# Performance work log

Measured on AMD Instinct MI355X. Metric: run time of the kernel, lower is better.

## Reference

```python
import jax, jax.numpy as jnp
import numpy as np
import math

D_MODEL = 1024
N_HEADS = 16
D_HEAD = D_MODEL // N_HEADS
MAX_SEQ_LEN = 2048
BASE = 10000.0


def _rope_tables(L):
    pos = jnp.arange(L, dtype=jnp.float32)[:, None]                      # [L,1]
    freqs = jnp.exp(-math.log(BASE) * jnp.arange(0, D_HEAD, 2, dtype=jnp.float32) / D_HEAD)  # [d/2]
    angles = pos * freqs                                                  # [L, d/2]
    return jnp.sin(angles), jnp.cos(angles)


def _apply_rope(x, sin, cos):
    # x: [B, L, H, d_head], interleaved even/odd rotation
    s = sin[None, :, None, :]
    c = cos[None, :, None, :]
    x_even, x_odd = x[..., ::2], x[..., 1::2]
    rot_even = x_even * c - x_odd * s
    rot_odd = x_even * s + x_odd * c
    # re-interleave: stack on new last axis then flatten
    return jnp.stack([rot_even, rot_odd], axis=-1).reshape(x.shape)


def setup_inputs() -> dict:
    key = jax.random.key(0)
    k0, k1, k2, k3, k4 = jax.random.split(key, 5)
    B, L = 2, 2048
    scale = 1.0 / math.sqrt(D_MODEL)
    return {
        "x": jax.random.normal(k0, (B, L, D_MODEL), dtype=jnp.float32),
        "W_q": jax.random.normal(k1, (D_MODEL, D_MODEL), dtype=jnp.float32) * scale,
        "W_k": jax.random.normal(k2, (D_MODEL, D_MODEL), dtype=jnp.float32) * scale,
        "W_v": jax.random.normal(k3, (D_MODEL, D_MODEL), dtype=jnp.float32) * scale,
        "W_o": jax.random.normal(k4, (D_MODEL, D_MODEL), dtype=jnp.float32) * scale,
    }


def reference(x, W_q, W_k, W_v, W_o):
    B, L, _ = x.shape
    sin, cos = _rope_tables(L)
    # nn.Linear(no bias): y = x @ W.T
    q = (x @ W_q.T).reshape(B, L, N_HEADS, D_HEAD)
    k = (x @ W_k.T).reshape(B, L, N_HEADS, D_HEAD)
    v = (x @ W_v.T).reshape(B, L, N_HEADS, D_HEAD)
    q = _apply_rope(q, sin, cos)
    k = _apply_rope(k, sin, cos)
    scores = jnp.einsum('blhd,bshd->bhls', q, k) / math.sqrt(D_HEAD)
    weights = jax.nn.softmax(scores, axis=-1)
    out = jnp.einsum('bhls,bshd->blhd', weights, v).reshape(B, L, D_MODEL)
    return out @ W_o.T
```

## Files before the change

kernel.cpp:

```cpp
#include <hip/hip_runtime.h>
#include <hip/hip_bf16.h>
#include <math.h>

typedef __bf16 bf16_t;
typedef __bf16 bf16x8 __attribute__((ext_vector_type(8)));
typedef __bf16 bf16x4 __attribute__((ext_vector_type(4)));
typedef float  f32x4  __attribute__((ext_vector_type(4)));
typedef float  f32x16 __attribute__((ext_vector_type(16)));
typedef unsigned u32x4 __attribute__((ext_vector_type(4)));

#define D_MODEL 1024
#define NH      16
#define DH      64
#define LSEQ    2048
#define NROWS   4096
#define LOG2E   1.44269504088896340736f
#define SHIFT_L2 17.312340490667562f

__device__ __forceinline__ void gld_lds16(bf16_t* lds, const bf16_t* g) {
  __builtin_amdgcn_global_load_lds(
      (__attribute__((address_space(1))) void*)(unsigned long long)g,
      (__attribute__((address_space(3))) void*)lds,
      16, 0, 0);
}

__device__ __forceinline__ unsigned cvtpk_bf16(float lo, float hi) {
  unsigned r;
  asm("v_cvt_pk_bf16_f32 %0, %1, %2" : "=v"(r) : "v"(lo), "v"(hi));
  return r;
}

__device__ __forceinline__ void pl32swap(unsigned& a, unsigned& b) {
  asm volatile("v_permlane32_swap_b32 %0, %1" : "+v"(a), "+v"(b));
}

__global__ __launch_bounds__(256)
void k_prep(const float* __restrict__ x,
            const float* __restrict__ w0, const float* __restrict__ w1,
            const float* __restrict__ w2, const float* __restrict__ w3,
            bf16_t* __restrict__ xb, bf16_t* __restrict__ wout, float2* __restrict__ tab)
{
  int gid = blockIdx.x * 256 + threadIdx.x;
  if (gid < 1048576) {
    float4 v = ((const float4*)x)[gid];
    bf16x4 o = { (bf16_t)v.x, (bf16_t)v.y, (bf16_t)v.z, (bf16_t)v.w };
    ((bf16x4*)xb)[gid] = o;
  } else if (gid < 2097152) {
    int i = gid - 1048576;
    int src = i >> 18;
    const float* w = (src == 0) ? w0 : (src == 1) ? w1 : (src == 2) ? w2 : w3;
    float4 v = ((const float4*)w)[i & 262143];
    bf16x4 o = { (bf16_t)v.x, (bf16_t)v.y, (bf16_t)v.z, (bf16_t)v.w };
    ((bf16x4*)wout)[i] = o;
  } else if (gid < 2162688) {
    int i = gid - 2097152;
    int l = i >> 5, p = i & 31;
    float freq = expf(-0.28782313662425575f * (float)p);
    float s, c;
    sincosf((float)l * freq, &s, &c);
    tab[i] = make_float2(c, s);
  }
}

template<int MODE>
__global__ __launch_bounds__(512, 6)
void k_gemm(const bf16_t* __restrict__ A, const bf16_t* __restrict__ B,
            int N, int K,
            float* __restrict__ Fo,
            bf16_t* __restrict__ Qo, bf16_t* __restrict__ Ko, bf16_t* __restrict__ Vo,
            const float2* __restrict__ tab)
{
  __shared__ bf16_t As[3][128 * 32];
  __shared__ bf16_t Bs[3][128 * 32];
  const int tid  = threadIdx.x;
  const int wave = tid >> 6, lane = tid & 63;
  const int hi   = lane >> 4, lo = lane & 15;
  const int m0   = blockIdx.y * 128, n0 = blockIdx.x * 128;
  const int wr2  = (wave >> 1) * 32, wc2 = (wave & 1) * 64;

  const int srow = tid >> 2, sslot = tid & 3;
  const bf16_t* Ap = A + (size_t)(m0 + srow) * K + (sslot ^ ((srow >> 1) & 3)) * 8;
  const bf16_t* Bp = B + (size_t)(n0 + srow) * K + (sslot ^ ((srow >> 1) & 3)) * 8;

  auto stage = [&](int buf) {
    gld_lds16(&As[buf][tid * 8], Ap);
    gld_lds16(&Bs[buf][tid * 8], Bp);
    Ap += 32; Bp += 32;
  };

  const int s16 = (hi ^ ((lo >> 1) & 3)) * 8;

  f32x4 acc[2][4] = {};

  auto compute = [&](int buf) {
    bf16x8 a[2], b[4];
    #pragma unroll
    for (int mi = 0; mi < 2; mi++)
      a[mi] = *(const bf16x8*)(&As[buf][(wr2 + mi * 16 + lo) * 32 + s16]);
    #pragma unroll
    for (int ni = 0; ni < 4; ni++)
      b[ni] = *(const bf16x8*)(&Bs[buf][(wc2 + ni * 16 + lo) * 32 + s16]);
    __builtin_amdgcn_s_setprio(1);
    #pragma unroll
    for (int mi = 0; mi < 2; mi++)
      #pragma unroll
      for (int ni = 0; ni < 4; ni++)
        acc[mi][ni] = __builtin_amdgcn_mfma_f32_16x16x32_bf16(a[mi], b[ni], acc[mi][ni], 0, 0, 0);
    __builtin_amdgcn_s_setprio(0);
  };

  const int nt = K >> 5;
  stage(0);
  stage(1);
  #pragma unroll 1
  for (int t = 0; t < nt - 2; ++t) {
    asm volatile("s_waitcnt vmcnt(2)" ::: "memory");
    __builtin_amdgcn_sched_barrier(0);
    __builtin_amdgcn_s_barrier();
    __builtin_amdgcn_sched_barrier(0);
    stage((t + 2) % 3);
    compute(t % 3);
  }
  asm volatile("s_waitcnt vmcnt(2)" ::: "memory");
  __builtin_amdgcn_sched_barrier(0);
  __builtin_amdgcn_s_barrier();
  __builtin_amdgcn_sched_barrier(0);
  compute((nt - 2) % 3);
  asm volatile("s_waitcnt vmcnt(0)" ::: "memory");
  __builtin_amdgcn_sched_barrier(0);
  __builtin_amdgcn_s_barrier();
  __builtin_amdgcn_sched_barrier(0);
  compute((nt - 1) % 3);

  if constexpr (MODE == 0) {
    #pragma unroll
    for (int mi = 0; mi < 2; mi++)
      #pragma unroll
      for (int ni = 0; ni < 4; ni++)
        #pragma unroll
        for (int r = 0; r < 4; r++) {
          int row = m0 + wr2 + mi * 16 + hi * 4 + r;
          int col = n0 + wc2 + ni * 16 + lo;
          Fo[(size_t)row * N + col] = acc[mi][ni][r];
        }
  } else {
    #pragma unroll
    for (int mi = 0; mi < 2; mi++)
      #pragma unroll
      for (int ni = 0; ni < 4; ni++)
        #pragma unroll
        for (int r = 0; r < 4; r++) {
          float val  = acc[mi][ni][r];
          float part = __shfl_xor(val, 1, 64);
          int row = m0 + wr2 + mi * 16 + hi * 4 + r;
          int col = n0 + wc2 + ni * 16 + lo;
          int which = col >> 10;
          int h = (col >> 6) & 15;
          int d = col & 63;
          int b = row >> 11, l = row & 2047;
          size_t oidx = ((size_t)(b * NH + h) * LSEQ + l) * DH + d;
          if (which == 2) {
            Vo[oidx] = (bf16_t)val;
          } else {
            float2 sc = tab[l * 32 + (d >> 1)];
            float rot = (d & 1) ? (part * sc.y + val * sc.x) : (val * sc.x - part * sc.y);
            if (which == 0) rot *= 0.125f * LOG2E;
            (which == 0 ? Qo : Ko)[oidx] = (bf16_t)rot;
          }
        }
  }
}

__global__ __launch_bounds__(256)
void k_vt(const bf16_t* __restrict__ Vrm, bf16_t* __restrict__ VT) {
  __shared__ bf16_t T[64][66];
  const int tid = threadIdx.x;
  const int bh = blockIdx.y, l0 = blockIdx.x * 64;
  const bf16_t* src = Vrm + ((size_t)bh * LSEQ + l0) * DH;
  #pragma unroll
  for (int pass = 0; pass < 2; pass++) {
    int chunk = tid + pass * 256;
    int row = chunk >> 3, slot = chunk & 7;
    bf16x8 v = *(const bf16x8*)(src + row * DH + slot * 8);
    #pragma unroll
    for (int j = 0; j < 8; j++) T[slot * 8 + j][row] = v[j];
  }
  __syncthreads();
  bf16_t* dst = VT + (size_t)bh * DH * LSEQ + l0;
  #pragma unroll
  for (int pass = 0; pass < 2; pass++) {
    int chunk = tid + pass * 256;
    int d = chunk >> 3, slot = chunk & 7;
    bf16x8 v;
    #pragma unroll
    for (int j = 0; j < 8; j++) v[j] = T[d][slot * 8 + j];
    *(bf16x8*)(dst + (size_t)d * LSEQ + slot * 8) = v;
  }
}

__global__ __launch_bounds__(1024)
void k_attn(const bf16_t* __restrict__ Q, const bf16_t* __restrict__ K,
            const bf16_t* __restrict__ VT, bf16_t* __restrict__ O)
{
  __shared__ __align__(16) bf16_t smem[49152];
  const int tid  = threadIdx.x;
  const int wave = tid >> 6, lane = tid & 63;
  const int kg   = wave & 1;
  const int qg   = wave >> 1;
  const int ql   = lane & 31;
  const int hi   = lane >> 5;
  const int bh = blockIdx.x;
  const int qblock = blockIdx.y * 256 + qg * 32;

  bf16_t* kbase = smem + kg * 3 * 4096;
  bf16_t* vbase = smem + 24576 + kg * 3 * 4096;

  const bf16_t* Qb = Q + (size_t)bh * LSEQ * DH;

  bf16x8 qf[4];
  #pragma unroll
  for (int s = 0; s < 4; s++)
    qf[s] = *(const bf16x8*)(Qb + (size_t)(qblock + ql) * DH + s * 16 + hi * 8);

  const int r0 = qg * 8 + (lane >> 3), s0l = lane & 7;
  const int swo = (s0l ^ (r0 & 7)) * 8;
  const bf16_t* kgp = K  + ((size_t)bh * LSEQ + kg * 1024 + r0) * DH + swo;
  const bf16_t* vgp = VT + ((size_t)bh * DH + r0) * LSEQ + kg * 1024 + swo;
  const int dstoff = qg * 512 + lane * 8;

  auto stage = [&](int buf) {
    gld_lds16(kbase + buf * 4096 + dstoff, kgp);
    gld_lds16(vbase + buf * 4096 + dstoff, vgp);
    kgp += 64 * DH; vgp += 64;
  };

  f32x16 acc[2] = {};
  float lrun = 0.f;

  f32x16 shinit;
  #pragma unroll
  for (int r = 0; r < 16; r++) shinit[r] = -SHIFT_L2;

  auto compute = [&](const bf16_t* Kbuf, const bf16_t* Vbuf) {
    const char* Kcur = (const char*)Kbuf;
    f32x16 st[2] = { shinit, shinit };
    __builtin_amdgcn_s_setprio(1);
    #pragma unroll
    for (int kt = 0; kt < 2; kt++) {
      int row = kt * 32 + ql;
      int swz = (row & 7) << 4;
      #pragma unroll
      for (int s = 0; s < 4; s++) {
        bf16x8 ka = *(const bf16x8*)(Kcur + row * 128 + ((s * 32 + hi * 16) ^ swz));
        st[kt] = __builtin_amdgcn_mfma_f32_32x32x16_bf16(ka, qf[s], st[kt], 0, 0, 0);
      }
    }
    __builtin_amdgcn_s_setprio(0);

    float p[32];
    float rs = 0.f;
    #pragma unroll
    for (int kt = 0; kt < 2; kt++)
      #pragma unroll
      for (int r = 0; r < 16; r++) {
        float e = __builtin_amdgcn_exp2f(st[kt][r]);
        p[kt * 16 + r] = e;
        rs += e;
      }
    lrun += rs;

    bf16x8 pa[4];
    #pragma unroll
    for (int g = 0; g < 4; g++) {
      unsigned a0 = cvtpk_bf16(p[g * 8 + 0], p[g * 8 + 1]);
      unsigned b0 = cvtpk_bf16(p[g * 8 + 4], p[g * 8 + 5]);
      pl32swap(a0, b0);
      unsigned a1 = cvtpk_bf16(p[g * 8 + 2], p[g * 8 + 3]);
      unsigned b1 = cvtpk_bf16(p[g * 8 + 6], p[g * 8 + 7]);
      pl32swap(a1, b1);
      union { u32x4 u; bf16x8 h; } w;
      w.u[0] = a0; w.u[1] = a1; w.u[2] = b0; w.u[3] = b1;
      pa[g] = w.h;
    }

    const char* Vcur = (const char*)Vbuf;
    __builtin_amdgcn_s_setprio(1);
    #pragma unroll
    for (int dt = 0; dt < 2; dt++) {
      int row = dt * 32 + ql;
      int swz = (row & 7) << 4;
      #pragma unroll
      for (int ks = 0; ks < 4; ks++) {
        bf16x8 va = *(const bf16x8*)(Vcur + row * 128 + ((ks * 32 + hi * 16) ^ swz));
        acc[dt] = __builtin_amdgcn_mfma_f32_32x32x16_bf16(va, pa[ks], acc[dt], 0, 0, 0);
      }
    }
    __builtin_amdgcn_s_setprio(0);
  };

  stage(0);
  stage(1);
  #pragma unroll 1
  for (int t = 0; t < 14; ++t) {
    asm volatile("s_waitcnt vmcnt(2)" ::: "memory");
    __builtin_amdgcn_sched_barrier(0);
    __builtin_amdgcn_s_barrier();
    __builtin_amdgcn_sched_barrier(0);
    stage((t + 2) % 3);
    compute(kbase + (t % 3) * 4096, vbase + (t % 3) * 4096);
  }
  asm volatile("s_waitcnt vmcnt(2)" ::: "memory");
  __builtin_amdgcn_sched_barrier(0);
  __builtin_amdgcn_s_barrier();
  __builtin_amdgcn_sched_barrier(0);
  compute(kbase + 2 * 4096, vbase + 2 * 4096);
  asm volatile("s_waitcnt vmcnt(0)" ::: "memory");
  __builtin_amdgcn_sched_barrier(0);
  __builtin_amdgcn_s_barrier();
  __builtin_amdgcn_sched_barrier(0);
  compute(kbase, vbase);

  __syncthreads();
  float* xch = (float*)smem;
  float* px = xch + (qg * 64 + lane) * 34;
  if (kg == 1) {
    #pragma unroll
    for (int r = 0; r < 16; r++) { px[r] = acc[0][r]; px[16 + r] = acc[1][r]; }
    px[32] = lrun;
  }
  __syncthreads();
  if (kg == 0) {
    #pragma unroll
    for (int r = 0; r < 16; r++) { acc[0][r] += px[r]; acc[1][r] += px[16 + r]; }
    lrun += px[32];
    float lfull = lrun + __shfl_xor(lrun, 32, 64);
    float inv = 1.0f / lfull;
    const int b = bh >> 4, h = bh & 15;
    const int lpos = qblock + ql;
    #pragma unroll
    for (int dt = 0; dt < 2; dt++)
      #pragma unroll
      for (int r = 0; r < 16; r++) {
        int d = dt * 32 + (r & 3) + 8 * (r >> 2) + 4 * hi;
        O[(size_t)(b * LSEQ + lpos) * D_MODEL + h * DH + d] = (bf16_t)(acc[dt][r] * inv);
      }
  }
}

extern "C" void kernel_launch(void* const* d_in, const int* in_sizes, int n_in,
                              void* d_out, int out_size, void* d_ws, size_t ws_size,
                              hipStream_t stream)
{
  (void)in_sizes; (void)n_in; (void)out_size; (void)ws_size;
  const float* x  = (const float*)d_in[0];
  const float* Wq = (const float*)d_in[1];
  const float* Wk = (const float*)d_in[2];
  const float* Wv = (const float*)d_in[3];
  const float* Wo = (const float*)d_in[4];
  float* out = (float*)d_out;

  bf16_t* ws   = (bf16_t*)d_ws;
  bf16_t* xb   = ws;
  bf16_t* wqkv = xb + (size_t)NROWS * D_MODEL;
  bf16_t* wo   = wqkv + (size_t)3 * D_MODEL * D_MODEL;
  bf16_t* Qw   = wo + (size_t)D_MODEL * D_MODEL;
  bf16_t* Kw   = Qw + (size_t)NROWS * D_MODEL;
  bf16_t* Vw   = Kw + (size_t)NROWS * D_MODEL;
  bf16_t* VTw  = Vw + (size_t)NROWS * D_MODEL;
  bf16_t* Aw   = VTw + (size_t)NROWS * D_MODEL;
  float2* tab  = (float2*)(Aw + (size_t)NROWS * D_MODEL);

  k_prep<<<8448, 256, 0, stream>>>(x, Wq, Wk, Wv, Wo, xb, wqkv, tab);

  dim3 g1(3072 / 128, 4096 / 128);
  k_gemm<1><<<g1, 512, 0, stream>>>(xb, wqkv, 3072, 1024, nullptr, Qw, Kw, Vw, tab);

  dim3 gv(LSEQ / 64, 32);
  k_vt<<<gv, 256, 0, stream>>>(Vw, VTw);

  dim3 g2(32, LSEQ / 256);
  k_attn<<<g2, 1024, 0, stream>>>(Qw, Kw, VTw, Aw);

  dim3 g3(1024 / 128, 4096 / 128);
  k_gemm<0><<<g3, 512, 0, stream>>>(Aw, wo, 1024, 1024, out, nullptr, nullptr, nullptr, nullptr);
}
```

Before: 117.4 us.

## Split GEMM K-loop across wave pairs with 64x64 warp tiles and LDS reduction

Each wave now owns a 64x64 output tile instead of 32x64, and paired waves alternate K-steps (split-K within the block). The partial accumulators are reduced through LDS before the epilogue. The aim is fewer LDS fragment loads per MFMA, through better register-level reuse of A and B. In exchange, accumulator registers double, occupancy drops (launch bounds 6 to 4), LDS grows to 72KB, half the waves idle during each compute step, and a reduction pass is added.

```diff
diff --git a/kernel.cpp b/kernel.cpp
--- a/kernel.cpp
+++ b/kernel.cpp
@@ -63,46 +63,51 @@
 }
 
 template<int MODE>
-__global__ __launch_bounds__(512, 6)
+__global__ __launch_bounds__(512, 4)
 void k_gemm(const bf16_t* __restrict__ A, const bf16_t* __restrict__ B,
             int N, int K,
             float* __restrict__ Fo,
             bf16_t* __restrict__ Qo, bf16_t* __restrict__ Ko, bf16_t* __restrict__ Vo,
             const float2* __restrict__ tab)
 {
-  __shared__ bf16_t As[3][128 * 32];
-  __shared__ bf16_t Bs[3][128 * 32];
+  __shared__ __align__(16) char smem[73728];
   const int tid  = threadIdx.x;
   const int wave = tid >> 6, lane = tid & 63;
   const int hi   = lane >> 4, lo = lane & 15;
   const int m0   = blockIdx.y * 128, n0 = blockIdx.x * 128;
-  const int wr2  = (wave >> 1) * 32, wc2 = (wave & 1) * 64;
+  const int pos  = wave >> 1, ks = wave & 1;
+  const int wr2  = (pos >> 1) * 64, wc2 = (pos & 1) * 64;
+
+  auto Asb = [&](int b) { return (bf16_t*)(smem + b * 8192); };
+  auto Bsb = [&](int b) { return (bf16_t*)(smem + 24576 + b * 8192); };
 
   const int srow = tid >> 2, sslot = tid & 3;
   const bf16_t* Ap = A + (size_t)(m0 + srow) * K + (sslot ^ ((srow >> 1) & 3)) * 8;
   const bf16_t* Bp = B + (size_t)(n0 + srow) * K + (sslot ^ ((srow >> 1) & 3)) * 8;
 
   auto stage = [&](int buf) {
-    gld_lds16(&As[buf][tid * 8], Ap);
-    gld_lds16(&Bs[buf][tid * 8], Bp);
+    gld_lds16(Asb(buf) + tid * 8, Ap);
+    gld_lds16(Bsb(buf) + tid * 8, Bp);
     Ap += 32; Bp += 32;
   };
 
   const int s16 = (hi ^ ((lo >> 1) & 3)) * 8;
 
-  f32x4 acc[2][4] = {};
+  f32x4 acc[4][4] = {};
 
   auto compute = [&](int buf) {
-    bf16x8 a[2], b[4];
-    #pragma unroll
-    for (int mi = 0; mi < 2; mi++)
-      a[mi] = *(const bf16x8*)(&As[buf][(wr2 + mi * 16 + lo) * 32 + s16]);
+    const bf16_t* Ac = Asb(buf);
+    const bf16_t* Bc = Bsb(buf);
+    bf16x8 a[4], b[4];
+    #pragma unroll
+    for (int mi = 0; mi < 4; mi++)
+      a[mi] = *(const bf16x8*)(Ac + (wr2 + mi * 16 + lo) * 32 + s16);
     #pragma unroll
     for (int ni = 0; ni < 4; ni++)
-      b[ni] = *(const bf16x8*)(&Bs[buf][(wc2 + ni * 16 + lo) * 32 + s16]);
+      b[ni] = *(const bf16x8*)(Bc + (wc2 + ni * 16 + lo) * 32 + s16);
     __builtin_amdgcn_s_setprio(1);
     #pragma unroll
-    for (int mi = 0; mi < 2; mi++)
+    for (int mi = 0; mi < 4; mi++)
       #pragma unroll
       for (int ni = 0; ni < 4; ni++)
         acc[mi][ni] = __builtin_amdgcn_mfma_f32_16x16x32_bf16(a[mi], b[ni], acc[mi][ni], 0, 0, 0);
@@ -119,55 +124,77 @@
     __builtin_amdgcn_s_barrier();
     __builtin_amdgcn_sched_barrier(0);
     stage((t + 2) % 3);
-    compute(t % 3);
+    if ((t & 1) == ks) compute(t % 3);
   }
   asm volatile("s_waitcnt vmcnt(2)" ::: "memory");
   __builtin_amdgcn_sched_barrier(0);
   __builtin_amdgcn_s_barrier();
   __builtin_amdgcn_sched_barrier(0);
-  compute((nt - 2) % 3);
+  if (((nt - 2) & 1) == ks) compute((nt - 2) % 3);
   asm volatile("s_waitcnt vmcnt(0)" ::: "memory");
   __builtin_amdgcn_sched_barrier(0);
   __builtin_amdgcn_s_barrier();
   __builtin_amdgcn_sched_barrier(0);
-  compute((nt - 1) % 3);
-
-  if constexpr (MODE == 0) {
-    #pragma unroll
-    for (int mi = 0; mi < 2; mi++)
+  if (((nt - 1) & 1) == ks) compute((nt - 1) % 3);
+
+  __syncthreads();
+  float* px = (float*)smem + ((size_t)(pos * 64 + lane)) * 65;
+  if (ks == 1) {
+    #pragma unroll
+    for (int mi = 0; mi < 4; mi++)
       #pragma unroll
       for (int ni = 0; ni < 4; ni++)
         #pragma unroll
-        for (int r = 0; r < 4; r++) {
-          int row = m0 + wr2 + mi * 16 + hi * 4 + r;
-          int col = n0 + wc2 + ni * 16 + lo;
-          Fo[(size_t)row * N + col] = acc[mi][ni][r];
-        }
-  } else {
-    #pragma unroll
-    for (int mi = 0; mi < 2; mi++)
+        for (int r = 0; r < 4; r++)
+          px[mi * 16 + ni * 4 + r] = acc[mi][ni][r];
+  }
+  __syncthreads();
+  if (ks == 0) {
+    #pragma unroll
+    for (int mi = 0; mi < 4; mi++)
       #pragma unroll
       for (int ni = 0; ni < 4; ni++)
         #pragma unroll
-        for (int r = 0; r < 4; r++) {
-          float val  = acc[mi][ni][r];
-          float part = __shfl_xor(val, 1, 64);
-          int row = m0 + wr2 + mi * 16 + hi * 4 + r;
-          int col = n0 + wc2 + ni * 16 + lo;
-          int which = col >> 10;
-          int h = (col >> 6) & 15;
-          int d = col & 63;
-          int b = row >> 11, l = row & 2047;
-          size_t oidx = ((size_t)(b * NH + h) * LSEQ + l) * DH + d;
-          if (which == 2) {
-            Vo[oidx] = (bf16_t)val;
-          } else {
-            float2 sc = tab[l * 32 + (d >> 1)];
-            float rot = (d & 1) ? (part * sc.y + val * sc.x) : (val * sc.x - part * sc.y);
-            if (which == 0) rot *= 0.125f * LOG2E;
-            (which == 0 ? Qo : Ko)[oidx] = (bf16_t)rot;
+        for (int r = 0; r < 4; r++)
+          acc[mi][ni][r] += px[mi * 16 + ni * 4 + r];
+
+    if constexpr (MODE == 0) {
+      #pragma unroll
+      for (int mi = 0; mi < 4; mi++)
+        #pragma unroll
+        for (int ni = 0; ni < 4; ni++)
+          #pragma unroll
+          for (int r = 0; r < 4; r++) {
+            int row = m0 + wr2 + mi * 16 + hi * 4 + r;
+            int col = n0 + wc2 + ni * 16 + lo;
+            Fo[(size_t)row * N + col] = acc[mi][ni][r];
           }
-        }
+    } else {
+      #pragma unroll
+      for (int mi = 0; mi < 4; mi++)
+        #pragma unroll
+        for (int ni = 0; ni < 4; ni++)
+          #pragma unroll
+          for (int r = 0; r < 4; r++) {
+            float val  = acc[mi][ni][r];
+            float part = __shfl_xor(val, 1, 64);
+            int row = m0 + wr2 + mi * 16 + hi * 4 + r;
+            int col = n0 + wc2 + ni * 16 + lo;
+            int which = col >> 10;
+            int h = (col >> 6) & 15;
+            int d = col & 63;
+            int b = row >> 11, l = row & 2047;
+            size_t oidx = ((size_t)(b * NH + h) * LSEQ + l) * DH + d;
+            if (which == 2) {
+              Vo[oidx] = (bf16_t)val;
+            } else {
+              float2 sc = tab[l * 32 + (d >> 1)];
+              float rot = (d & 1) ? (part * sc.y + val * sc.x) : (val * sc.x - part * sc.y);
+              if (which == 0) rot *= 0.125f * LOG2E;
+              (which == 0 ? Qo : Ko)[oidx] = (bf16_t)rot;
+            }
+          }
+    }
   }
 }
 
```

New measurement: 146.5 us. 24.8% more time.
